# Kernel tuning notes

Hardware: AMD Instinct MI355X
Metric: run time of the kernel (lower is better)

## Reference

```python
import jax, jax.numpy as jnp
import numpy as np

HIDDEN = 256
HEADS = 1
HEAD_DIM = HIDDEN // HEADS  # internal_dim == hidden (downsample_rate=1)
SQ = 4096        # 64x64 current-frame tokens
N_MEM = 4        # memory frames
N_OBJ = 64       # object-pointer tokens excluded from RoPE
SK = N_MEM * SQ + N_OBJ  # 16448


def _rotate_pairwise(x):
    # [x0, x1, x2, x3, ...] -> [-x1, x0, -x3, x2, ...]
    s = x.shape
    x = x.reshape(s[:-1] + (s[-1] // 2, 2))
    return jnp.stack([-x[..., 1], x[..., 0]], axis=-1).reshape(s)


def setup_inputs() -> dict:
    key = jax.random.key(0)
    ks = jax.random.split(key, 16)
    d = {}
    d["query"] = jax.random.normal(ks[0], (1, 1, SQ, HIDDEN), jnp.float32)
    d["key"] = jax.random.normal(ks[1], (1, 1, SK, HIDDEN), jnp.float32)
    d["value"] = jax.random.normal(ks[2], (1, 1, SK, HIDDEN), jnp.float32)
    # rotary tables broadcast over (B*P, heads) like in the keras code
    d["cos"] = jax.random.uniform(ks[3], (1, 1, SQ, HEAD_DIM), jnp.float32, -1.0, 1.0)
    d["sin"] = jax.random.uniform(ks[4], (1, 1, SQ, HEAD_DIM), jnp.float32, -1.0, 1.0)
    w = 0.02
    d["q_w"] = jax.random.normal(ks[5], (HIDDEN, HIDDEN), jnp.float32) * w
    d["q_b"] = jnp.zeros((HIDDEN,), jnp.float32)
    d["k_w"] = jax.random.normal(ks[6], (HIDDEN, HIDDEN), jnp.float32) * w
    d["k_b"] = jnp.zeros((HIDDEN,), jnp.float32)
    d["v_w"] = jax.random.normal(ks[7], (HIDDEN, HIDDEN), jnp.float32) * w
    d["v_b"] = jnp.zeros((HIDDEN,), jnp.float32)
    d["o_w"] = jax.random.normal(ks[8], (HIDDEN, HIDDEN), jnp.float32) * w
    d["o_b"] = jnp.zeros((HIDDEN,), jnp.float32)
    d["num_k_exclude_rope"] = N_OBJ
    return d


def reference(query, key, value, cos, sin, q_w, q_b, k_w, k_b, v_w, v_b, o_w, o_b, num_k_exclude_rope):
    B, P, Sq, _ = query.shape
    Sk = key.shape[2]
    nex = int(num_k_exclude_rope)

    def heads(x):  # (B,P,S,internal) -> (B*P, H, S, hd)
        s = x.shape
        return x.reshape(s[0] * s[1], s[2], HEADS, HEAD_DIM).transpose(0, 2, 1, 3)

    q = heads(query @ q_w + q_b)
    k = heads(key @ k_w + k_b)
    v = heads(value @ v_w + v_b)

    # 2D rotary embedding (fp32 math, as in the original)
    qf = q.astype(jnp.float32)
    q_emb = (qf * cos + _rotate_pairwise(qf) * sin).astype(q.dtype)

    k_rot = k[:, :, :Sk - nex, :]
    k_pass = k[:, :, Sk - nex:, :] if nex > 0 else None
    if k_rot.shape[2] != Sq:  # rope_k_repeat=True path
        rf = k_rot.shape[2] // Sq
        cos_k = jnp.repeat(cos, rf, axis=2)
        sin_k = jnp.repeat(sin, rf, axis=2)
    else:
        cos_k, sin_k = cos, sin
    kf = k_rot.astype(jnp.float32)
    k_emb = (kf * cos_k + _rotate_pairwise(kf) * sin_k).astype(k.dtype)
    if k_pass is not None:
        k_emb = jnp.concatenate([k_emb, k_pass], axis=2)

    scaling = HEAD_DIM ** -0.5
    scores = jnp.einsum('bhqd,bhkd->bhqk', q_emb, k_emb) * scaling
    attn = jax.nn.softmax(scores, axis=-1)
    out = jnp.einsum('bhqk,bhkd->bhqd', attn, v)  # (B*P, H, Sq, hd)
    out = out.transpose(0, 2, 1, 3).reshape(B, P, Sq, HEADS * HEAD_DIM)
    return out @ o_w + o_b
```

## Files before the change

### kernel.cpp

```cpp
#include <hip/hip_runtime.h>
#include <stdint.h>

typedef _Float16 half_t;
typedef __attribute__((ext_vector_type(8))) _Float16 f16x8;
typedef __attribute__((ext_vector_type(4))) _Float16 f16x4;
typedef __attribute__((ext_vector_type(4))) float f32x4;

#define SQN 4096
#define SKN 16448
#define NROPE 16384
#define NSPLIT 8
#define NTILES 514
#define SCQ 0.090168441360f

#define GLD16(gp, lp) __builtin_amdgcn_global_load_lds( \
    (const __attribute__((address_space(1))) void*)(const void*)(gp), \
    (__attribute__((address_space(3))) void*)(void*)(lp), 16, 0, 0)

__global__ __launch_bounds__(256) void wt_kernel(const float* __restrict__ qw,
    const float* __restrict__ kw, const float* __restrict__ vw, const float* __restrict__ ow,
    half_t* __restrict__ wt)
{
    __shared__ float tile[64][65];
    int b = blockIdx.x;
    int mat = b >> 4, t4 = b & 15;
    int k0 = (t4 >> 2) << 6, n0 = (t4 & 3) << 6;
    const float* W = (mat == 0) ? qw : (mat == 1) ? kw : (mat == 2) ? vw : ow;
    half_t* WT = wt + mat * 65536;
    int t = threadIdx.x;
#pragma unroll
    for (int j = 0; j < 16; ++j) {
        int e = j * 256 + t;
        tile[e >> 6][e & 63] = W[(k0 + (e >> 6)) * 256 + n0 + (e & 63)];
    }
    __syncthreads();
#pragma unroll
    for (int j = 0; j < 16; ++j) {
        int e = j * 256 + t;
        WT[(n0 + (e >> 6)) * 256 + k0 + (e & 63)] = (half_t)tile[e & 63][e >> 6];
    }
}

__global__ __launch_bounds__(256) void proj_kernel(
    const float* __restrict__ query, const float* __restrict__ key, const float* __restrict__ value,
    const float* __restrict__ cosp, const float* __restrict__ sinp,
    const half_t* __restrict__ wt,
    const float* __restrict__ qb, const float* __restrict__ kb, const float* __restrict__ vb,
    half_t* __restrict__ Qe, half_t* __restrict__ Ke, half_t* __restrict__ VTb)
{
    __shared__ __align__(16) half_t S[64 * 264];

    int b = blockIdx.x;
    int mode; long row0;
    const float* X; const half_t* W; const float* bias;
    if (b < 64)       { mode = 0; row0 = (long)b * 64;         X = query; W = wt;           bias = qb; }
    else if (b < 321) { mode = 1; row0 = (long)(b - 64) * 64;  X = key;   W = wt + 65536;   bias = kb; }
    else              { mode = 2; row0 = (long)(b - 321) * 64; X = value; W = wt + 131072;  bias = vb; }

    int tid = threadIdx.x;
    int w = tid >> 6, l = tid & 63;
    int l16 = l & 15, l4 = l >> 4;
    long rw0 = row0 + w * 16;

    f32x4 acc[16];
#pragma unroll
    for (int i = 0; i < 16; ++i) acc[i] = (f32x4){0.f, 0.f, 0.f, 0.f};

    const float* xrow = X + (rw0 + l16) * 256;
    for (int ks = 0; ks < 8; ++ks) {
        f32x4 xa = *reinterpret_cast<const f32x4*>(xrow + ks * 32 + l4 * 8);
        f32x4 xb = *reinterpret_cast<const f32x4*>(xrow + ks * 32 + l4 * 8 + 4);
        f16x8 af;
#pragma unroll
        for (int j = 0; j < 4; ++j) { af[j] = (half_t)xa[j]; af[4 + j] = (half_t)xb[j]; }
#pragma unroll
        for (int nt = 0; nt < 16; ++nt) {
            f16x8 bf = *reinterpret_cast<const f16x8*>(W + (nt * 16 + l16) * 256 + ks * 32 + l4 * 8);
            acc[nt] = __builtin_amdgcn_mfma_f32_16x16x32_f16(af, bf, acc[nt], 0, 0, 0);
        }
    }

    bool dorope = (mode == 0) || (mode == 1 && row0 < NROPE);
#pragma unroll
    for (int nt = 0; nt < 16; ++nt) {
        int d = nt * 16 + l16;
        float bv = bias[d];
        f32x4 v = acc[nt];
#pragma unroll
        for (int r = 0; r < 4; ++r) v[r] += bv;
        if (dorope) {
#pragma unroll
            for (int r = 0; r < 4; ++r) {
                long m = rw0 + l4 * 4 + r;
                long crow = (mode == 0) ? m : (m >> 2);
                float c = cosp[crow * 256 + d];
                float s = sinp[crow * 256 + d];
                float val = v[r];
                float other = __shfl_xor(val, 1);
                float rot = (d & 1) ? other : -other;
                v[r] = val * c + rot * s;
                if (mode == 0) v[r] *= SCQ;
            }
        }
        if (mode == 2) {
            long kv = rw0 + l4 * 4;
            long kvb = kv >> 5;
            int  kvw = (int)(kv & 31);
            f16x4 pk;
#pragma unroll
            for (int r = 0; r < 4; ++r) pk[r] = (half_t)v[r];
            *reinterpret_cast<f16x4*>(VTb + kvb * 8192 + (long)d * 32 + kvw) = pk;
        } else {
            int wrow = w * 16 + l4 * 4;
#pragma unroll
            for (int r = 0; r < 4; ++r)
                S[(wrow + r) * 264 + d] = (half_t)v[r];
        }
    }

    if (mode != 2) {
        __syncthreads();
        half_t* O = ((mode == 0) ? Qe : Ke) + row0 * 256;
#pragma unroll
        for (int i = 0; i < 8; ++i) {
            int e = (i * 256 + tid) * 8;
            int row = e >> 8, col = e & 255;
            f16x8 val = *reinterpret_cast<const f16x8*>(&S[row * 264 + col]);
            *reinterpret_cast<f16x8*>(O + e) = val;
        }
    }
}

__global__ __launch_bounds__(256, 2) void flash_kernel(
    const half_t* __restrict__ Qe, const half_t* __restrict__ Ke, const half_t* __restrict__ VTb,
    half_t* __restrict__ AOp, float* __restrict__ Lse)
{
    __shared__ __align__(16) half_t Ks[2][32 * 256];
    __shared__ __align__(16) half_t Vs[2][256 * 32];
    __shared__ __align__(16) half_t Ps[4][16 * 40];

    int b = blockIdx.x;
    int chunk = b & 7;
    int qb = b >> 3;
    int tid = threadIdx.x;
    int w = tid >> 6, l = tid & 63;
    int l16 = l & 15, l4 = l >> 4;
    long qw0 = (long)qb * 64 + w * 16;

    int t0 = (NTILES * chunk) / NSPLIT;
    int t1 = (NTILES * (chunk + 1)) / NSPLIT;

    f16x8 qf[8];
#pragma unroll
    for (int ks = 0; ks < 8; ++ks)
        qf[ks] = *reinterpret_cast<const f16x8*>(Qe + (qw0 + l16) * 256 + ks * 32 + l4 * 8);

    f32x4 o[16];
#pragma unroll
    for (int i = 0; i < 16; ++i) o[i] = (f32x4){0.f, 0.f, 0.f, 0.f};
    float mrun = -3.0e38f;
    float lsum = 0.0f;

#define STAGE(d_, t) do {                                                    \
        const half_t* kb_ = Ke + (long)(t) * 8192;                           \
        const half_t* vb_ = VTb + (long)(t) * 8192;                          \
        half_t* ksd = &Ks[d_][0];                                            \
        half_t* vsd = &Vs[d_][0];                                            \
        _Pragma("unroll")                                                    \
        for (int j = 0; j < 4; ++j) {                                        \
            int pb = w * 4096 + j * 1024;                                    \
            int p  = pb + l * 16;                                            \
            int row = p >> 9;                                                \
            int cols = ((p >> 4) & 31) ^ (row & 7);                          \
            GLD16(kb_ + row * 256 + cols * 8, ksd + (pb >> 1));              \
            GLD16(vb_ + (p >> 1), vsd + (pb >> 1));                          \
        }                                                                    \
    } while (0)

    STAGE(0, t0);
    asm volatile("s_waitcnt vmcnt(0)" ::: "memory");
    __builtin_amdgcn_s_barrier();

    half_t* Pw = Ps[w];
    const int xk = l16 & 7;
    int cur = 0;

    for (int t = t0; t < t1; ++t) {
        if (t + 1 < t1) STAGE(cur ^ 1, t + 1);

        const half_t* KsC = &Ks[0][0] + cur * (32 * 256);
        const half_t* VsC = &Vs[0][0] + cur * (256 * 32);

        f32x4 s0 = (f32x4){0.f, 0.f, 0.f, 0.f};
        f32x4 s1 = (f32x4){0.f, 0.f, 0.f, 0.f};
#pragma unroll
        for (int ks = 0; ks < 8; ++ks) {
            int slot = ((ks * 4 + l4) ^ xk) << 3;
            f16x8 ka0 = *reinterpret_cast<const f16x8*>(KsC + l16 * 256 + slot);
            f16x8 ka1 = *reinterpret_cast<const f16x8*>(KsC + (16 + l16) * 256 + slot);
            s0 = __builtin_amdgcn_mfma_f32_16x16x32_f16(ka0, qf[ks], s0, 0, 0, 0);
            s1 = __builtin_amdgcn_mfma_f32_16x16x32_f16(ka1, qf[ks], s1, 0, 0, 0);
        }

        float tv[8];
#pragma unroll
        for (int r = 0; r < 4; ++r) { tv[r] = s0[r]; tv[4 + r] = s1[r]; }
        float pm = tv[0];
#pragma unroll
        for (int i = 1; i < 8; ++i) pm = fmaxf(pm, tv[i]);
        pm = fmaxf(pm, __shfl_xor(pm, 16));
        pm = fmaxf(pm, __shfl_xor(pm, 32));

        if (!__all(pm - mrun <= 8.0f)) {
            float mn = fmaxf(mrun, pm);
            float alpha = __builtin_amdgcn_exp2f(mrun - mn);
            lsum *= alpha;
            float ao[4];
#pragma unroll
            for (int r = 0; r < 4; ++r) ao[r] = __shfl(alpha, l4 * 4 + r);
#pragma unroll
            for (int i = 0; i < 16; ++i)
#pragma unroll
                for (int r = 0; r < 4; ++r) o[i][r] *= ao[r];
            mrun = mn;
        }

        float p[8];
        float psum = 0.f;
#pragma unroll
        for (int i = 0; i < 8; ++i) { p[i] = __builtin_amdgcn_exp2f(tv[i] - mrun); psum += p[i]; }
        psum += __shfl_xor(psum, 16);
        psum += __shfl_xor(psum, 32);
        lsum += psum;

        f16x4 pk0, pk1;
#pragma unroll
        for (int r = 0; r < 4; ++r) { pk0[r] = (half_t)p[r]; pk1[r] = (half_t)p[4 + r]; }
        *reinterpret_cast<f16x4*>(Pw + l16 * 40 + l4 * 4) = pk0;
        *reinterpret_cast<f16x4*>(Pw + l16 * 40 + 16 + l4 * 4) = pk1;

        f16x8 pa = *reinterpret_cast<const f16x8*>(Pw + l16 * 40 + l4 * 8);
#pragma unroll
        for (int nt = 0; nt < 16; ++nt) {
            f16x8 vbf = *reinterpret_cast<const f16x8*>(VsC + (nt * 16 + l16) * 32 + l4 * 8);
            o[nt] = __builtin_amdgcn_mfma_f32_16x16x32_f16(pa, vbf, o[nt], 0, 0, 0);
        }

        asm volatile("s_waitcnt vmcnt(0)" ::: "memory");
        __builtin_amdgcn_s_barrier();
        cur ^= 1;
    }
#undef STAGE

    float inv[4];
#pragma unroll
    for (int r = 0; r < 4; ++r) inv[r] = 1.0f / __shfl(lsum, l4 * 4 + r);
    half_t* Ab = AOp + ((long)chunk * SQN + qw0) * 256;
#pragma unroll
    for (int nt = 0; nt < 16; ++nt)
#pragma unroll
        for (int r = 0; r < 4; ++r)
            Ab[(l4 * 4 + r) * 256 + nt * 16 + l16] = (half_t)(o[nt][r] * inv[r]);
    if (l < 16)
        Lse[(long)chunk * SQN + qw0 + l16] = mrun + __builtin_amdgcn_logf(lsum);
}

__global__ __launch_bounds__(256) void oproj_kernel(
    const half_t* __restrict__ AOp, const float* __restrict__ Lse,
    const half_t* __restrict__ WTo, const float* __restrict__ ob,
    float* __restrict__ out)
{
    int b = blockIdx.x;
    int tid = threadIdx.x;
    int w = tid >> 6, l = tid & 63;
    int l16 = l & 15, l4 = l >> 4;
    long row = (long)b * 16 + l16;

    float ls[NSPLIT];
    float lmax = -3.0e38f;
#pragma unroll
    for (int c = 0; c < NSPLIT; ++c) { ls[c] = Lse[(long)c * SQN + row]; lmax = fmaxf(lmax, ls[c]); }
    float wgt[NSPLIT];
    float wsum = 0.f;
#pragma unroll
    for (int c = 0; c < NSPLIT; ++c) { wgt[c] = __builtin_amdgcn_exp2f(ls[c] - lmax); wsum += wgt[c]; }
    float invw = 1.0f / wsum;
#pragma unroll
    for (int c = 0; c < NSPLIT; ++c) wgt[c] *= invw;

    f32x4 acc[4];
#pragma unroll
    for (int i = 0; i < 4; ++i) acc[i] = (f32x4){0.f, 0.f, 0.f, 0.f};

#pragma unroll
    for (int ks = 0; ks < 8; ++ks) {
        float facc[8];
#pragma unroll
        for (int j = 0; j < 8; ++j) facc[j] = 0.f;
#pragma unroll
        for (int c = 0; c < NSPLIT; ++c) {
            f16x8 v = *reinterpret_cast<const f16x8*>(
                AOp + ((long)c * SQN + row) * 256 + ks * 32 + l4 * 8);
#pragma unroll
            for (int j = 0; j < 8; ++j) facc[j] += wgt[c] * (float)v[j];
        }
        f16x8 af;
#pragma unroll
        for (int j = 0; j < 8; ++j) af[j] = (half_t)facc[j];
#pragma unroll
        for (int nt = 0; nt < 4; ++nt) {
            f16x8 bf = *reinterpret_cast<const f16x8*>(
                WTo + ((w * 4 + nt) * 16 + l16) * 256 + ks * 32 + l4 * 8);
            acc[nt] = __builtin_amdgcn_mfma_f32_16x16x32_f16(af, bf, acc[nt], 0, 0, 0);
        }
    }

    long r0 = (long)b * 16;
#pragma unroll
    for (int nt = 0; nt < 4; ++nt) {
        int d = (w * 4 + nt) * 16 + l16;
        float bv = ob[d];
#pragma unroll
        for (int r = 0; r < 4; ++r)
            out[(r0 + l4 * 4 + r) * 256 + d] = acc[nt][r] + bv;
    }
}

extern "C" void kernel_launch(void* const* d_in, const int* in_sizes, int n_in,
                              void* d_out, int out_size, void* d_ws, size_t ws_size,
                              hipStream_t stream) {
    const float* query = (const float*)d_in[0];
    const float* key   = (const float*)d_in[1];
    const float* value = (const float*)d_in[2];
    const float* cosp  = (const float*)d_in[3];
    const float* sinp  = (const float*)d_in[4];
    const float* qw = (const float*)d_in[5];
    const float* qb = (const float*)d_in[6];
    const float* kw = (const float*)d_in[7];
    const float* kb = (const float*)d_in[8];
    const float* vw = (const float*)d_in[9];
    const float* vb = (const float*)d_in[10];
    const float* ow = (const float*)d_in[11];
    const float* ob = (const float*)d_in[12];

    char* ws = (char*)d_ws;
    half_t* Qe  = (half_t*)(ws);
    half_t* Ke  = (half_t*)(ws + 2097152);
    half_t* VTb = (half_t*)(ws + 10518528);
    half_t* WT  = (half_t*)(ws + 18939904);
    half_t* AOp = (half_t*)(ws + 19464192);
    float*  Lse = (float*)(ws + 36241408);

    hipLaunchKernelGGL(wt_kernel, dim3(64), dim3(256), 0, stream, qw, kw, vw, ow, WT);
    hipLaunchKernelGGL(proj_kernel, dim3(578), dim3(256), 0, stream,
                       query, key, value, cosp, sinp, WT, qb, kb, vb, Qe, Ke, VTb);
    hipLaunchKernelGGL(flash_kernel, dim3(512), dim3(256), 0, stream, Qe, Ke, VTb, AOp, Lse);
    hipLaunchKernelGGL(oproj_kernel, dim3(256), dim3(256), 0, stream, AOp, Lse, WT + 3 * 65536, ob, (float*)d_out);
}
```

Measured before the change: 188.4 us.

## Process two 16-row query tiles per wave and double the KV split count

Each wave now handles 32 query rows (two 16-row MFMA tiles) so every K/V tile staged in LDS is reused twice, halving K/V traffic per query. The block covers 128 queries, and the split-KV factor goes from 8 to 16 to keep the grid at 512 blocks; the Lse buffer is moved to fit the larger partial-output buffer. This costs double the accumulator registers (two sets of 64 f32 outputs), which under launch_bounds(256,2) may spill or cut occupancy, and the oproj merge must combine twice as many partials.

```diff
diff --git a/kernel.cpp b/kernel.cpp
--- a/kernel.cpp
+++ b/kernel.cpp
@@ -9,7 +9,7 @@
 #define SQN 4096
 #define SKN 16448
 #define NROPE 16384
-#define NSPLIT 8
+#define NSPLIT 16
 #define NTILES 514
 #define SCQ 0.090168441360f
 
@@ -137,29 +137,34 @@
 {
     __shared__ __align__(16) half_t Ks[2][32 * 256];
     __shared__ __align__(16) half_t Vs[2][256 * 32];
-    __shared__ __align__(16) half_t Ps[4][16 * 40];
+    __shared__ __align__(16) half_t Ps[4][2][16 * 40];
 
     int b = blockIdx.x;
-    int chunk = b & 7;
-    int qb = b >> 3;
+    int chunk = b & 15;
+    int qb = b >> 4;
     int tid = threadIdx.x;
     int w = tid >> 6, l = tid & 63;
     int l16 = l & 15, l4 = l >> 4;
-    long qw0 = (long)qb * 64 + w * 16;
+    long qw0 = (long)qb * 128 + w * 32;
 
     int t0 = (NTILES * chunk) / NSPLIT;
     int t1 = (NTILES * (chunk + 1)) / NSPLIT;
 
-    f16x8 qf[8];
-#pragma unroll
-    for (int ks = 0; ks < 8; ++ks)
-        qf[ks] = *reinterpret_cast<const f16x8*>(Qe + (qw0 + l16) * 256 + ks * 32 + l4 * 8);
-
-    f32x4 o[16];
-#pragma unroll
-    for (int i = 0; i < 16; ++i) o[i] = (f32x4){0.f, 0.f, 0.f, 0.f};
-    float mrun = -3.0e38f;
-    float lsum = 0.0f;
+    f16x8 qf0[8], qf1[8];
+#pragma unroll
+    for (int ks = 0; ks < 8; ++ks) {
+        qf0[ks] = *reinterpret_cast<const f16x8*>(Qe + (qw0 + l16) * 256 + ks * 32 + l4 * 8);
+        qf1[ks] = *reinterpret_cast<const f16x8*>(Qe + (qw0 + 16 + l16) * 256 + ks * 32 + l4 * 8);
+    }
+
+    f32x4 o0[16], o1[16];
+#pragma unroll
+    for (int i = 0; i < 16; ++i) {
+        o0[i] = (f32x4){0.f, 0.f, 0.f, 0.f};
+        o1[i] = (f32x4){0.f, 0.f, 0.f, 0.f};
+    }
+    float mrun0 = -3.0e38f, lsum0 = 0.0f;
+    float mrun1 = -3.0e38f, lsum1 = 0.0f;
 
 #define STAGE(d_, t) do {                                                    \
         const half_t* kb_ = Ke + (long)(t) * 8192;                           \
@@ -181,7 +186,8 @@
     asm volatile("s_waitcnt vmcnt(0)" ::: "memory");
     __builtin_amdgcn_s_barrier();
 
-    half_t* Pw = Ps[w];
+    half_t* Pw0 = &Ps[w][0][0];
+    half_t* Pw1 = &Ps[w][1][0];
     const int xk = l16 & 7;
     int cur = 0;
 
@@ -191,59 +197,99 @@
         const half_t* KsC = &Ks[0][0] + cur * (32 * 256);
         const half_t* VsC = &Vs[0][0] + cur * (256 * 32);
 
-        f32x4 s0 = (f32x4){0.f, 0.f, 0.f, 0.f};
-        f32x4 s1 = (f32x4){0.f, 0.f, 0.f, 0.f};
+        f32x4 s00 = (f32x4){0.f, 0.f, 0.f, 0.f};
+        f32x4 s01 = (f32x4){0.f, 0.f, 0.f, 0.f};
+        f32x4 s10 = (f32x4){0.f, 0.f, 0.f, 0.f};
+        f32x4 s11 = (f32x4){0.f, 0.f, 0.f, 0.f};
 #pragma unroll
         for (int ks = 0; ks < 8; ++ks) {
             int slot = ((ks * 4 + l4) ^ xk) << 3;
             f16x8 ka0 = *reinterpret_cast<const f16x8*>(KsC + l16 * 256 + slot);
             f16x8 ka1 = *reinterpret_cast<const f16x8*>(KsC + (16 + l16) * 256 + slot);
-            s0 = __builtin_amdgcn_mfma_f32_16x16x32_f16(ka0, qf[ks], s0, 0, 0, 0);
-            s1 = __builtin_amdgcn_mfma_f32_16x16x32_f16(ka1, qf[ks], s1, 0, 0, 0);
-        }
-
-        float tv[8];
-#pragma unroll
-        for (int r = 0; r < 4; ++r) { tv[r] = s0[r]; tv[4 + r] = s1[r]; }
-        float pm = tv[0];
-#pragma unroll
-        for (int i = 1; i < 8; ++i) pm = fmaxf(pm, tv[i]);
-        pm = fmaxf(pm, __shfl_xor(pm, 16));
-        pm = fmaxf(pm, __shfl_xor(pm, 32));
-
-        if (!__all(pm - mrun <= 8.0f)) {
-            float mn = fmaxf(mrun, pm);
-            float alpha = __builtin_amdgcn_exp2f(mrun - mn);
-            lsum *= alpha;
-            float ao[4];
-#pragma unroll
-            for (int r = 0; r < 4; ++r) ao[r] = __shfl(alpha, l4 * 4 + r);
-#pragma unroll
-            for (int i = 0; i < 16; ++i)
-#pragma unroll
-                for (int r = 0; r < 4; ++r) o[i][r] *= ao[r];
-            mrun = mn;
-        }
-
-        float p[8];
-        float psum = 0.f;
-#pragma unroll
-        for (int i = 0; i < 8; ++i) { p[i] = __builtin_amdgcn_exp2f(tv[i] - mrun); psum += p[i]; }
-        psum += __shfl_xor(psum, 16);
-        psum += __shfl_xor(psum, 32);
-        lsum += psum;
-
-        f16x4 pk0, pk1;
-#pragma unroll
-        for (int r = 0; r < 4; ++r) { pk0[r] = (half_t)p[r]; pk1[r] = (half_t)p[4 + r]; }
-        *reinterpret_cast<f16x4*>(Pw + l16 * 40 + l4 * 4) = pk0;
-        *reinterpret_cast<f16x4*>(Pw + l16 * 40 + 16 + l4 * 4) = pk1;
-
-        f16x8 pa = *reinterpret_cast<const f16x8*>(Pw + l16 * 40 + l4 * 8);
+            s00 = __builtin_amdgcn_mfma_f32_16x16x32_f16(ka0, qf0[ks], s00, 0, 0, 0);
+            s01 = __builtin_amdgcn_mfma_f32_16x16x32_f16(ka1, qf0[ks], s01, 0, 0, 0);
+            s10 = __builtin_amdgcn_mfma_f32_16x16x32_f16(ka0, qf1[ks], s10, 0, 0, 0);
+            s11 = __builtin_amdgcn_mfma_f32_16x16x32_f16(ka1, qf1[ks], s11, 0, 0, 0);
+        }
+
+        {
+            float tv[8];
+#pragma unroll
+            for (int r = 0; r < 4; ++r) { tv[r] = s00[r]; tv[4 + r] = s01[r]; }
+            float pm = tv[0];
+#pragma unroll
+            for (int i = 1; i < 8; ++i) pm = fmaxf(pm, tv[i]);
+            pm = fmaxf(pm, __shfl_xor(pm, 16));
+            pm = fmaxf(pm, __shfl_xor(pm, 32));
+            if (!__all(pm - mrun0 <= 8.0f)) {
+                float mn = fmaxf(mrun0, pm);
+                float alpha = __builtin_amdgcn_exp2f(mrun0 - mn);
+                lsum0 *= alpha;
+                float ao[4];
+#pragma unroll
+                for (int r = 0; r < 4; ++r) ao[r] = __shfl(alpha, l4 * 4 + r);
+#pragma unroll
+                for (int i = 0; i < 16; ++i)
+#pragma unroll
+                    for (int r = 0; r < 4; ++r) o0[i][r] *= ao[r];
+                mrun0 = mn;
+            }
+            float p[8];
+            float psum = 0.f;
+#pragma unroll
+            for (int i = 0; i < 8; ++i) { p[i] = __builtin_amdgcn_exp2f(tv[i] - mrun0); psum += p[i]; }
+            psum += __shfl_xor(psum, 16);
+            psum += __shfl_xor(psum, 32);
+            lsum0 += psum;
+            f16x4 pk0, pk1;
+#pragma unroll
+            for (int r = 0; r < 4; ++r) { pk0[r] = (half_t)p[r]; pk1[r] = (half_t)p[4 + r]; }
+            *reinterpret_cast<f16x4*>(Pw0 + l16 * 40 + l4 * 4) = pk0;
+            *reinterpret_cast<f16x4*>(Pw0 + l16 * 40 + 16 + l4 * 4) = pk1;
+        }
+        {
+            float tv[8];
+#pragma unroll
+            for (int r = 0; r < 4; ++r) { tv[r] = s10[r]; tv[4 + r] = s11[r]; }
+            float pm = tv[0];
+#pragma unroll
+            for (int i = 1; i < 8; ++i) pm = fmaxf(pm, tv[i]);
+            pm = fmaxf(pm, __shfl_xor(pm, 16));
+            pm = fmaxf(pm, __shfl_xor(pm, 32));
+            if (!__all(pm - mrun1 <= 8.0f)) {
+                float mn = fmaxf(mrun1, pm);
+                float alpha = __builtin_amdgcn_exp2f(mrun1 - mn);
+                lsum1 *= alpha;
+                float ao[4];
+#pragma unroll
+                for (int r = 0; r < 4; ++r) ao[r] = __shfl(alpha, l4 * 4 + r);
+#pragma unroll
+                for (int i = 0; i < 16; ++i)
+#pragma unroll
+                    for (int r = 0; r < 4; ++r) o1[i][r] *= ao[r];
+                mrun1 = mn;
+            }
+            float p[8];
+            float psum = 0.f;
+#pragma unroll
+            for (int i = 0; i < 8; ++i) { p[i] = __builtin_amdgcn_exp2f(tv[i] - mrun1); psum += p[i]; }
+            psum += __shfl_xor(psum, 16);
+            psum += __shfl_xor(psum, 32);
+            lsum1 += psum;
+            f16x4 pk0, pk1;
+#pragma unroll
+            for (int r = 0; r < 4; ++r) { pk0[r] = (half_t)p[r]; pk1[r] = (half_t)p[4 + r]; }
+            *reinterpret_cast<f16x4*>(Pw1 + l16 * 40 + l4 * 4) = pk0;
+            *reinterpret_cast<f16x4*>(Pw1 + l16 * 40 + 16 + l4 * 4) = pk1;
+        }
+
+        f16x8 pa0 = *reinterpret_cast<const f16x8*>(Pw0 + l16 * 40 + l4 * 8);
+        f16x8 pa1 = *reinterpret_cast<const f16x8*>(Pw1 + l16 * 40 + l4 * 8);
 #pragma unroll
         for (int nt = 0; nt < 16; ++nt) {
             f16x8 vbf = *reinterpret_cast<const f16x8*>(VsC + (nt * 16 + l16) * 32 + l4 * 8);
-            o[nt] = __builtin_amdgcn_mfma_f32_16x16x32_f16(pa, vbf, o[nt], 0, 0, 0);
+            o0[nt] = __builtin_amdgcn_mfma_f32_16x16x32_f16(pa0, vbf, o0[nt], 0, 0, 0);
+            o1[nt] = __builtin_amdgcn_mfma_f32_16x16x32_f16(pa1, vbf, o1[nt], 0, 0, 0);
         }
 
         asm volatile("s_waitcnt vmcnt(0)" ::: "memory");
@@ -252,17 +298,32 @@
     }
 #undef STAGE
 
-    float inv[4];
-#pragma unroll
-    for (int r = 0; r < 4; ++r) inv[r] = 1.0f / __shfl(lsum, l4 * 4 + r);
-    half_t* Ab = AOp + ((long)chunk * SQN + qw0) * 256;
-#pragma unroll
-    for (int nt = 0; nt < 16; ++nt)
-#pragma unroll
-        for (int r = 0; r < 4; ++r)
-            Ab[(l4 * 4 + r) * 256 + nt * 16 + l16] = (half_t)(o[nt][r] * inv[r]);
-    if (l < 16)
-        Lse[(long)chunk * SQN + qw0 + l16] = mrun + __builtin_amdgcn_logf(lsum);
+    {
+        float inv[4];
+#pragma unroll
+        for (int r = 0; r < 4; ++r) inv[r] = 1.0f / __shfl(lsum0, l4 * 4 + r);
+        half_t* Ab = AOp + ((long)chunk * SQN + qw0) * 256;
+#pragma unroll
+        for (int nt = 0; nt < 16; ++nt)
+#pragma unroll
+            for (int r = 0; r < 4; ++r)
+                Ab[(l4 * 4 + r) * 256 + nt * 16 + l16] = (half_t)(o0[nt][r] * inv[r]);
+        if (l < 16)
+            Lse[(long)chunk * SQN + qw0 + l16] = mrun0 + __builtin_amdgcn_logf(lsum0);
+    }
+    {
+        float inv[4];
+#pragma unroll
+        for (int r = 0; r < 4; ++r) inv[r] = 1.0f / __shfl(lsum1, l4 * 4 + r);
+        half_t* Ab = AOp + ((long)chunk * SQN + qw0 + 16) * 256;
+#pragma unroll
+        for (int nt = 0; nt < 16; ++nt)
+#pragma unroll
+            for (int r = 0; r < 4; ++r)
+                Ab[(l4 * 4 + r) * 256 + nt * 16 + l16] = (half_t)(o1[nt][r] * inv[r]);
+        if (l < 16)
+            Lse[(long)chunk * SQN + qw0 + 16 + l16] = mrun1 + __builtin_amdgcn_logf(lsum1);
+    }
 }
 
 __global__ __launch_bounds__(256) void oproj_kernel(
@@ -349,7 +410,7 @@
     half_t* VTb = (half_t*)(ws + 10518528);
     half_t* WT  = (half_t*)(ws + 18939904);
     half_t* AOp = (half_t*)(ws + 19464192);
-    float*  Lse = (float*)(ws + 36241408);
+    float*  Lse = (float*)(ws + 53018624);
 
     hipLaunchKernelGGL(wt_kernel, dim3(64), dim3(256), 0, stream, qw, kw, vw, ow, WT);
     hipLaunchKernelGGL(proj_kernel, dim3(578), dim3(256), 0, stream,
```

After: 216.5 us. 14.9% more time.

## Single-buffer V tile and raise flash split to 12 chunks at 3 blocks/CU

Applied to the files above, without the earlier changes.

The flash kernel's V shared-memory tile becomes single-buffered, which shrinks LDS per block so three blocks can reside per CU. The key split rises from 8 to 12 chunks, giving a 768-block grid that fills 256 CUs at 3 blocks each. The next V tile is now loaded only after the PV MFMAs finish, behind an extra barrier, so that load is no longer overlapped with compute. Other blocks on the CU are meant to hide that latency. The partial-output buffer grows and the Lse offset is moved to match.

```diff
diff --git a/kernel.cpp b/kernel.cpp
--- a/kernel.cpp
+++ b/kernel.cpp
@@ -9,7 +9,7 @@
 #define SQN 4096
 #define SKN 16448
 #define NROPE 16384
-#define NSPLIT 8
+#define NSPLIT 12
 #define NTILES 514
 #define SCQ 0.090168441360f
 
@@ -131,17 +131,17 @@
     }
 }
 
-__global__ __launch_bounds__(256, 2) void flash_kernel(
+__global__ __launch_bounds__(256, 3) void flash_kernel(
     const half_t* __restrict__ Qe, const half_t* __restrict__ Ke, const half_t* __restrict__ VTb,
     half_t* __restrict__ AOp, float* __restrict__ Lse)
 {
     __shared__ __align__(16) half_t Ks[2][32 * 256];
-    __shared__ __align__(16) half_t Vs[2][256 * 32];
+    __shared__ __align__(16) half_t Vs[256 * 32];
     __shared__ __align__(16) half_t Ps[4][16 * 40];
 
     int b = blockIdx.x;
-    int chunk = b & 7;
-    int qb = b >> 3;
+    int chunk = b % NSPLIT;
+    int qb = b / NSPLIT;
     int tid = threadIdx.x;
     int w = tid >> 6, l = tid & 63;
     int l16 = l & 15, l4 = l >> 4;
@@ -161,11 +161,9 @@
     float mrun = -3.0e38f;
     float lsum = 0.0f;
 
-#define STAGE(d_, t) do {                                                    \
+#define STAGE_K(d_, t) do {                                                  \
         const half_t* kb_ = Ke + (long)(t) * 8192;                           \
-        const half_t* vb_ = VTb + (long)(t) * 8192;                          \
         half_t* ksd = &Ks[d_][0];                                            \
-        half_t* vsd = &Vs[d_][0];                                            \
         _Pragma("unroll")                                                    \
         for (int j = 0; j < 4; ++j) {                                        \
             int pb = w * 4096 + j * 1024;                                    \
@@ -173,11 +171,20 @@
             int row = p >> 9;                                                \
             int cols = ((p >> 4) & 31) ^ (row & 7);                          \
             GLD16(kb_ + row * 256 + cols * 8, ksd + (pb >> 1));              \
-            GLD16(vb_ + (p >> 1), vsd + (pb >> 1));                          \
         }                                                                    \
     } while (0)
-
-    STAGE(0, t0);
+#define STAGE_V(t) do {                                                      \
+        const half_t* vb_ = VTb + (long)(t) * 8192;                          \
+        _Pragma("unroll")                                                    \
+        for (int j = 0; j < 4; ++j) {                                        \
+            int pb = w * 4096 + j * 1024;                                    \
+            int p  = pb + l * 16;                                            \
+            GLD16(vb_ + (p >> 1), Vs + (pb >> 1));                           \
+        }                                                                    \
+    } while (0)
+
+    STAGE_K(0, t0);
+    STAGE_V(t0);
     asm volatile("s_waitcnt vmcnt(0)" ::: "memory");
     __builtin_amdgcn_s_barrier();
 
@@ -186,10 +193,10 @@
     int cur = 0;
 
     for (int t = t0; t < t1; ++t) {
-        if (t + 1 < t1) STAGE(cur ^ 1, t + 1);
+        bool more = (t + 1 < t1);
+        if (more) STAGE_K(cur ^ 1, t + 1);
 
         const half_t* KsC = &Ks[0][0] + cur * (32 * 256);
-        const half_t* VsC = &Vs[0][0] + cur * (256 * 32);
 
         f32x4 s0 = (f32x4){0.f, 0.f, 0.f, 0.f};
         f32x4 s1 = (f32x4){0.f, 0.f, 0.f, 0.f};
@@ -242,15 +249,18 @@
         f16x8 pa = *reinterpret_cast<const f16x8*>(Pw + l16 * 40 + l4 * 8);
 #pragma unroll
         for (int nt = 0; nt < 16; ++nt) {
-            f16x8 vbf = *reinterpret_cast<const f16x8*>(VsC + (nt * 16 + l16) * 32 + l4 * 8);
+            f16x8 vbf = *reinterpret_cast<const f16x8*>(Vs + (nt * 16 + l16) * 32 + l4 * 8);
             o[nt] = __builtin_amdgcn_mfma_f32_16x16x32_f16(pa, vbf, o[nt], 0, 0, 0);
         }
 
+        __builtin_amdgcn_s_barrier();
+        if (more) STAGE_V(t + 1);
         asm volatile("s_waitcnt vmcnt(0)" ::: "memory");
         __builtin_amdgcn_s_barrier();
         cur ^= 1;
     }
-#undef STAGE
+#undef STAGE_K
+#undef STAGE_V
 
     float inv[4];
 #pragma unroll
@@ -349,11 +359,11 @@
     half_t* VTb = (half_t*)(ws + 10518528);
     half_t* WT  = (half_t*)(ws + 18939904);
     half_t* AOp = (half_t*)(ws + 19464192);
-    float*  Lse = (float*)(ws + 36241408);
+    float*  Lse = (float*)(ws + 44630016);
 
     hipLaunchKernelGGL(wt_kernel, dim3(64), dim3(256), 0, stream, qw, kw, vw, ow, WT);
     hipLaunchKernelGGL(proj_kernel, dim3(578), dim3(256), 0, stream,
                        query, key, value, cosp, sinp, WT, qb, kb, vb, Qe, Ke, VTb);
-    hipLaunchKernelGGL(flash_kernel, dim3(512), dim3(256), 0, stream, Qe, Ke, VTb, AOp, Lse);
+    hipLaunchKernelGGL(flash_kernel, dim3(768), dim3(256), 0, stream, Qe, Ke, VTb, AOp, Lse);
     hipLaunchKernelGGL(oproj_kernel, dim3(256), dim3(256), 0, stream, AOp, Lse, WT + 3 * 65536, ob, (float*)d_out);
 }
```

Result: slower. 247.5 us (+31.4%).
